# Performance work log

Measured on AMD Instinct MI355X. Metric: run time of the kernel, lower is better.

The kernel has to match this reference:

```python
import jax, jax.numpy as jnp
import numpy as np

EPS = 1e-10
ENTROPY_COEF = 0.1
COLSUM_COEF = 1.0


def setup_inputs() -> dict:
    key = jax.random.key(0)
    k1, k2, k3 = jax.random.split(key, 3)
    H, T, B, S = 512, 50003, 32, 256
    colsum_threshold = 0.5
    return {
        "text_input": jax.random.randint(k1, (B, S), 0, T, dtype=jnp.int32),
        "init_logits": jnp.zeros((H,), dtype=jnp.float32),
        "transition_logits": jax.random.normal(k2, (H, H), dtype=jnp.float32) * 0.1,
        "emission_logits": jax.random.normal(k3, (H, T), dtype=jnp.float32) * 0.1,
        "colsum_threshold": colsum_threshold,
    }


def reference(text_input, init_logits, transition_logits, emission_logits, colsum_threshold):
    # softmax-normalized HMM parameters
    text_pi = jax.nn.softmax(init_logits, axis=0)              # [H]
    text_A = jax.nn.softmax(transition_logits, axis=1)         # [H,H]
    text_B = jax.nn.softmax(emission_logits, axis=1)           # [H,T]

    log_pi = jnp.log(text_pi + EPS)                            # [H]
    log_A = jnpp = jnp.log(text_A + EPS)                       # [H,H]
    log_B = jnp.log(text_B + EPS)                              # [H,T]

    # gather per-token emission log-probs: [B,S,H]
    log_B_obs = log_B.T[text_input]

    # t = 0
    log_alpha0 = log_pi[None, :] + log_B_obs[:, 0, :]          # [B,H]

    def step(log_alpha, obs_t):
        # logsumexp over source state i: [B,H(i),1] + [1,H(i),H(j)] -> [B,H(j)]
        trans = log_alpha[:, :, None] + log_A[None, :, :]
        new_alpha = jax.nn.logsumexp(trans, axis=1) + obs_t
        return new_alpha, None

    obs_rest = jnp.swapaxes(log_B_obs[:, 1:, :], 0, 1)         # [S-1,B,H]
    log_alpha_final, _ = jax.lax.scan(step, log_alpha0, obs_rest)

    log_likelihood = jax.nn.logsumexp(log_alpha_final, axis=1)  # [B]
    likelihood_loss = -jnp.mean(log_likelihood)

    transition_entropy = -jnp.sum(text_A * jnp.log(text_A + EPS), axis=1)
    transition_entropy_loss = jnp.mean(transition_entropy) * ENTROPY_COEF

    col_sums = jnp.sum(text_A, axis=0)
    colsum_reg = jnp.sum(jax.nn.relu(colsum_threshold - col_sums)) * COLSUM_COEF

    hmm_loss = likelihood_loss + transition_entropy_loss + colsum_reg
    return text_pi, text_A, text_B, hmm_loss
```

## Files before the change

### kernel.cpp

```cpp
#include <hip/hip_runtime.h>
#include <hip/hip_bf16.h>
#include <stdint.h>

#define HH 512
#define BB 32
#define SSEQ 256
#define TVOC 50003
#define EPSF 1e-10f
#define EMSCALE 96.0f
#define TOTLOG 2759.2459164008406f

typedef float f32x4 __attribute__((ext_vector_type(4)));
typedef int v8i __attribute__((ext_vector_type(8)));

__device__ __forceinline__ float wave_max(float v) {
#pragma unroll
  for (int off = 32; off; off >>= 1) v = fmaxf(v, __shfl_xor(v, off));
  return v;
}
__device__ __forceinline__ float wave_sum(float v) {
#pragma unroll
  for (int off = 32; off; off >>= 1) v += __shfl_xor(v, off);
  return v;
}

__global__ __launch_bounds__(512) void init_ws_kernel(float* ws) {
  if (threadIdx.x < 8) ws[threadIdx.x] = 0.0f;
  ws[8 + threadIdx.x] = 0.0f;
}

__global__ __launch_bounds__(512) void softmax_pi_kernel(
    const float* __restrict__ x, float* __restrict__ pi) {
  const int tid = threadIdx.x;
  const int wv = tid >> 6, ln = tid & 63;
  __shared__ float red[8];
  float v = x[tid];
  float m = wave_max(v);
  if (ln == 0) red[wv] = m;
  __syncthreads();
  float M = red[0];
#pragma unroll
  for (int i = 1; i < 8; ++i) M = fmaxf(M, red[i]);
  float e = __expf(v - M);
  float s = wave_sum(e);
  __syncthreads();
  if (ln == 0) red[wv] = s;
  __syncthreads();
  float S = 0.f;
#pragma unroll
  for (int i = 0; i < 8; ++i) S += red[i];
  pi[tid] = e / S;
}

__global__ __launch_bounds__(512) void softmaxA_kernel(
    const float* __restrict__ tl, float* __restrict__ outA,
    float* __restrict__ ws_ent) {
  const int r = blockIdx.x, tid = threadIdx.x;
  const int wv = tid >> 6, ln = tid & 63;
  __shared__ float red[8];
  float v = tl[(size_t)r * HH + tid];
  float m = wave_max(v);
  if (ln == 0) red[wv] = m;
  __syncthreads();
  float M = red[0];
#pragma unroll
  for (int i = 1; i < 8; ++i) M = fmaxf(M, red[i]);
  float e = __expf(v - M);
  float s = wave_sum(e);
  __syncthreads();
  if (ln == 0) red[wv] = s;
  __syncthreads();
  float S = 0.f;
#pragma unroll
  for (int i = 0; i < 8; ++i) S += red[i];
  float p = e / S;
  outA[(size_t)r * HH + tid] = p;
  float ent = -p * __logf(p + EPSF);
  ent = wave_sum(ent);
  __syncthreads();
  if (ln == 0) red[wv] = ent;
  __syncthreads();
  if (tid == 0) {
    float tot = 0.f;
#pragma unroll
    for (int i = 0; i < 8; ++i) tot += red[i];
    atomicAdd(ws_ent, tot);
  }
}

__global__ __launch_bounds__(512) void colsum_partial_kernel(
    const float* __restrict__ outA, float* __restrict__ col) {
  const int j = threadIdx.x;
  const int i0 = blockIdx.x * 64;
  float s = 0.f;
#pragma unroll 4
  for (int i = i0; i < i0 + 64; ++i) s += outA[(size_t)i * HH + j];
  atomicAdd(&col[j], s);
}

__global__ __launch_bounds__(1024) void softmaxB_gather_kernel(
    const float* __restrict__ el, float* __restrict__ outB,
    const int* __restrict__ tok, __hip_bfloat16* __restrict__ ems) {
  const int r = blockIdx.x, tid = threadIdx.x;
  const float* x = el + (size_t)r * TVOC;
  float* yo = outB + (size_t)r * TVOC;
  const int mis = (int)(((16u - ((unsigned)(uintptr_t)x & 15u)) & 15u) >> 2);
  const int body = (TVOC - mis) >> 2;
  const int tailoff = mis + body * 4;

  float m0 = -1e30f, s0 = 0.f, m1 = -1e30f, s1 = 0.f;
  float m2 = -1e30f, s2 = 0.f, m3 = -1e30f, s3 = 0.f;
  auto upd = [](float& m, float& s, float v) {
    if (v > m) { s = s * __expf(m - v) + 1.f; m = v; }
    else       { s += __expf(v - m); }
  };
  if (tid < mis) upd(m0, s0, x[tid]);
  const float4* x4 = (const float4*)(x + mis);
  for (int i = tid; i < body; i += 1024) {
    float4 v = x4[i];
    upd(m0, s0, v.x); upd(m1, s1, v.y); upd(m2, s2, v.z); upd(m3, s3, v.w);
  }
  for (int i = tailoff + tid; i < TVOC; i += 1024) upd(m0, s0, x[i]);
  auto mrg = [](float& m, float& s, float om, float os) {
    float nm = fmaxf(m, om);
    s = s * __expf(m - nm) + os * __expf(om - nm);
    m = nm;
  };
  mrg(m0, s0, m1, s1); mrg(m2, s2, m3, s3); mrg(m0, s0, m2, s2);
  float m = m0, s = s0;

#pragma unroll
  for (int off = 32; off; off >>= 1) {
    float om = __shfl_down(m, off), os = __shfl_down(s, off);
    float nm = fmaxf(m, om);
    s = s * __expf(m - nm) + os * __expf(om - nm);
    m = nm;
  }
  __shared__ float sm[16], ssv[16];
  __shared__ float bM, biZ;
  if ((tid & 63) == 0) { sm[tid >> 6] = m; ssv[tid >> 6] = s; }
  __syncthreads();
  if (tid == 0) {
    float M = sm[0], S = ssv[0];
#pragma unroll
    for (int w = 1; w < 16; ++w) {
      float nm = fmaxf(M, sm[w]);
      S = S * __expf(M - nm) + ssv[w] * __expf(sm[w] - nm);
      M = nm;
    }
    bM = M; biZ = 1.f / S;
  }
  __syncthreads();
  const float M = bM, iZ = biZ;
  if (tid < mis) yo[tid] = __expf(x[tid] - M) * iZ;
  float4* y4 = (float4*)(yo + mis);
  for (int i = tid; i < body; i += 1024) {
    float4 v = x4[i];
    float4 o;
    o.x = __expf(v.x - M) * iZ;
    o.y = __expf(v.y - M) * iZ;
    o.z = __expf(v.z - M) * iZ;
    o.w = __expf(v.w - M) * iZ;
    y4[i] = o;
  }
  for (int i = tailoff + tid; i < TVOC; i += 1024)
    yo[i] = __expf(x[i] - M) * iZ;

  const float gs = EMSCALE * iZ;
  const int rg = r >> 2, rl = r & 3;
  for (int idx = tid; idx < BB * SSEQ; idx += 1024) {
    const int sq = idx >> 5, b = idx & 31;
    const int t = tok[b * SSEQ + sq];
    ems[((size_t)(sq * 128 + rg) * 32 + b) * 4 + rl] =
        __float2bfloat16(__expf(x[t] - M) * gs);
  }
}

__global__ __launch_bounds__(512, 2) void scan_kernel(
    const float* __restrict__ d_pi, const float* __restrict__ d_A,
    const __hip_bfloat16* __restrict__ ems, float* __restrict__ ws_negll) {
  const int h = blockIdx.x;
  const int tid = threadIdx.x;
  const int lane = tid & 63;
  const int wave = tid >> 6;
  const int l15 = lane & 15;
  const int quad = lane >> 4;
  const int bG = h * 16 + l15;

  __shared__ __align__(16) unsigned char alpha[2][16][528];
  __shared__ float wmax[8][17];
  __shared__ float wsum[8][17];
  __shared__ float ls[16];

  const unsigned short* emsu = (const unsigned short*)ems;
  const uint2* emv = (const uint2*)ems;

  v8i aF[4][4];
#pragma unroll
  for (int n = 0; n < 4; ++n) {
    const int jg = wave * 64 + n * 16 + l15;
#pragma unroll
    for (int c = 0; c < 4; ++c) {
#pragma unroll
      for (int g = 0; g < 8; ++g) {
        const int k0 = c * 128 + quad * 32 + g * 4;
        const float v0 = d_A[(size_t)(k0 + 0) * HH + jg] * 512.0f;
        const float v1 = d_A[(size_t)(k0 + 1) * HH + jg] * 512.0f;
        const float v2 = d_A[(size_t)(k0 + 2) * HH + jg] * 512.0f;
        const float v3 = d_A[(size_t)(k0 + 3) * HH + jg] * 512.0f;
        int wrd = 0;
        wrd = __builtin_amdgcn_cvt_pk_fp8_f32(v0, v1, wrd, false);
        wrd = __builtin_amdgcn_cvt_pk_fp8_f32(v2, v3, wrd, true);
        aF[n][c][g] = wrd;
      }
    }
  }

#pragma unroll
  for (int it = 0; it < 2; ++it) {
    const int b = wave * 2 + it;
    const int bb = h * 16 + b;
    const int j0 = lane * 8;
    float vals[8];
    float m = -1e30f;
#pragma unroll
    for (int u = 0; u < 8; ++u) {
      const int j = j0 + u;
      const unsigned ew = (unsigned)emsu[((size_t)(j >> 2) * 32 + bb) * 4 + (j & 3)] << 16;
      vals[u] = (d_pi[j] + EPSF) * __uint_as_float(ew);
      m = fmaxf(m, vals[u]);
    }
    m = wave_max(m);
    if (lane == 0) ls[b] = __logf(m);
    const float r = 1.0f / m;
    int lo = 0, hi = 0;
    lo = __builtin_amdgcn_cvt_pk_fp8_f32(vals[0] * r, vals[1] * r, lo, false);
    lo = __builtin_amdgcn_cvt_pk_fp8_f32(vals[2] * r, vals[3] * r, lo, true);
    hi = __builtin_amdgcn_cvt_pk_fp8_f32(vals[4] * r, vals[5] * r, hi, false);
    hi = __builtin_amdgcn_cvt_pk_fp8_f32(vals[6] * r, vals[7] * r, hi, true);
    *(unsigned int*)&alpha[0][b][j0]     = (unsigned)lo;
    *(unsigned int*)&alpha[0][b][j0 + 4] = (unsigned)hi;
  }
  __syncthreads();

  const uint2* ep = emv + ((size_t)1 * 128 + wave * 16 + quad) * 32 + bG;
  uint2 evr[4];
#pragma unroll
  for (int n = 0; n < 4; ++n) evr[n] = ep[n * 128];
  ep += 128 * 32;

#pragma unroll 2
  for (int t = 1; t < SSEQ; ++t) {
    const int cur = (t - 1) & 1, nxt = t & 1;

    float ev[4][4];
#pragma unroll
    for (int n = 0; n < 4; ++n) {
      ev[n][0] = __uint_as_float(evr[n].x << 16);
      ev[n][1] = __uint_as_float(evr[n].x & 0xFFFF0000u);
      ev[n][2] = __uint_as_float(evr[n].y << 16);
      ev[n][3] = __uint_as_float(evr[n].y & 0xFFFF0000u);
    }
#pragma unroll
    for (int n = 0; n < 4; ++n) evr[n] = ep[n * 128];
    if (t <= SSEQ - 3) ep += 128 * 32;

    f32x4 acc0 = {0.f, 0.f, 0.f, 0.f}, acc1 = {0.f, 0.f, 0.f, 0.f};
    f32x4 acc2 = {0.f, 0.f, 0.f, 0.f}, acc3 = {0.f, 0.f, 0.f, 0.f};
#pragma unroll
    for (int c = 0; c < 4; ++c) {
      const unsigned char* ap = &alpha[cur][l15][c * 128 + quad * 32];
      v8i bf;
      *(int4*)&bf       = *(const int4*)ap;
      *(((int4*)&bf)+1) = *(const int4*)(ap + 16);
      acc0 = __builtin_amdgcn_mfma_scale_f32_16x16x128_f8f6f4(
          aF[0][c], bf, acc0, 0, 0, 0, 0x7F7F7F7F, 0, 0x7F7F7F7F);
      acc1 = __builtin_amdgcn_mfma_scale_f32_16x16x128_f8f6f4(
          aF[1][c], bf, acc1, 0, 0, 0, 0x7F7F7F7F, 0, 0x7F7F7F7F);
      acc2 = __builtin_amdgcn_mfma_scale_f32_16x16x128_f8f6f4(
          aF[2][c], bf, acc2, 0, 0, 0, 0x7F7F7F7F, 0, 0x7F7F7F7F);
      acc3 = __builtin_amdgcn_mfma_scale_f32_16x16x128_f8f6f4(
          aF[3][c], bf, acc3, 0, 0, 0, 0x7F7F7F7F, 0, 0x7F7F7F7F);
    }

    float y[4][4];
#pragma unroll
    for (int rg = 0; rg < 4; ++rg) {
      y[0][rg] = acc0[rg] * ev[0][rg];
      y[1][rg] = acc1[rg] * ev[1][rg];
      y[2][rg] = acc2[rg] * ev[2][rg];
      y[3][rg] = acc3[rg] * ev[3][rg];
    }

    float r = 1.0f;
    if ((t & 15) == 0) {
      float mm = -1e30f;
#pragma unroll
      for (int n = 0; n < 4; ++n)
#pragma unroll
        for (int rg = 0; rg < 4; ++rg) mm = fmaxf(mm, y[n][rg]);
      mm = fmaxf(mm, __shfl_xor(mm, 16));
      mm = fmaxf(mm, __shfl_xor(mm, 32));
      if (lane < 16) wmax[wave][lane] = mm;
      __syncthreads();
      float m = wmax[0][l15];
#pragma unroll
      for (int w = 1; w < 8; ++w) m = fmaxf(m, wmax[w][l15]);
      r = 1.0f / m;
      if (tid < 16) ls[tid] += __logf(m);
    }

#pragma unroll
    for (int n = 0; n < 4; ++n) {
      int d = 0;
      d = __builtin_amdgcn_cvt_pk_fp8_f32(y[n][0] * r, y[n][1] * r, d, false);
      d = __builtin_amdgcn_cvt_pk_fp8_f32(y[n][2] * r, y[n][3] * r, d, true);
      *(unsigned int*)&alpha[nxt][l15][wave * 64 + n * 16 + quad * 4] = (unsigned)d;
    }
    if (t == SSEQ - 1) {
      float s = 0.f;
#pragma unroll
      for (int n = 0; n < 4; ++n) s += y[n][0] + y[n][1] + y[n][2] + y[n][3];
      s *= r;
      s += __shfl_xor(s, 16);
      s += __shfl_xor(s, 32);
      if (lane < 16) wsum[wave][lane] = s;
    }
    __syncthreads();
  }

  if (wave == 0 && lane < 16) {
    float s = 0.f;
#pragma unroll
    for (int w = 0; w < 8; ++w) s += wsum[w][lane];
    const float LL = __logf(s) + ls[lane] - TOTLOG;
    atomicAdd(ws_negll, -LL * (1.0f / 32.0f));
  }
}

__global__ __launch_bounds__(512) void finalize_kernel(
    const float* __restrict__ ws, const float* __restrict__ col,
    const float* __restrict__ thr, float* __restrict__ out_loss) {
  const int j = threadIdx.x;
  float v = fmaxf(thr[0] - col[j], 0.f);
  v = wave_sum(v);
  __shared__ float red[8];
  if ((j & 63) == 0) red[j >> 6] = v;
  __syncthreads();
  if (j == 0) {
    float creg = 0.f;
#pragma unroll
    for (int i = 0; i < 8; ++i) creg += red[i];
    out_loss[0] = ws[1] + ws[0] * (0.1f / 512.0f) + creg;
  }
}

extern "C" void kernel_launch(void* const* d_in, const int* in_sizes, int n_in,
                              void* d_out, int out_size, void* d_ws, size_t ws_size,
                              hipStream_t stream) {
  const int*   tok    = (const int*)d_in[0];
  const float* initl  = (const float*)d_in[1];
  const float* transl = (const float*)d_in[2];
  const float* eml    = (const float*)d_in[3];
  const float* thr    = (const float*)d_in[4];

  float* out      = (float*)d_out;
  float* out_pi   = out;
  float* out_A    = out + HH;
  float* out_B    = out + HH + (size_t)HH * HH;
  float* out_loss = out + HH + (size_t)HH * HH + (size_t)HH * TVOC;

  float* wsf = (float*)d_ws;
  float* col = wsf + 8;
  __hip_bfloat16* ems = (__hip_bfloat16*)((char*)d_ws + 4096);

  init_ws_kernel<<<1, 512, 0, stream>>>(wsf);
  softmax_pi_kernel<<<1, 512, 0, stream>>>(initl, out_pi);
  softmaxA_kernel<<<512, 512, 0, stream>>>(transl, out_A, wsf + 0);
  colsum_partial_kernel<<<8, 512, 0, stream>>>(out_A, col);
  softmaxB_gather_kernel<<<512, 1024, 0, stream>>>(eml, out_B, tok, ems);
  scan_kernel<<<2, 512, 0, stream>>>(out_pi, out_A, ems, wsf + 1);
  finalize_kernel<<<1, 512, 0, stream>>>(wsf, col, thr, out_loss);
}
```

Measured before the change: 665.5 us.

## Split scan kernel across 16 waves per block with half the output columns each

The sequential HMM forward scan block grows from 8 to 16 waves. Each wave now owns 32 destination states (two MFMA accumulators) instead of 64, which halves the per-wave MFMA chain and the register-resident fp8 transition fragments on each serial step. The init step is also reworked to use vectorized loads of pi and emissions. In exchange, each per-step __syncthreads and the periodic max reduction now span 16 waves.

```diff
diff --git a/kernel.cpp b/kernel.cpp
--- a/kernel.cpp
+++ b/kernel.cpp
@@ -176,7 +176,7 @@
   }
 }
 
-__global__ __launch_bounds__(512, 2) void scan_kernel(
+__global__ __launch_bounds__(1024) void scan_kernel(
     const float* __restrict__ d_pi, const float* __restrict__ d_A,
     const __hip_bfloat16* __restrict__ ems, float* __restrict__ ws_negll) {
   const int h = blockIdx.x;
@@ -188,17 +188,16 @@
   const int bG = h * 16 + l15;
 
   __shared__ __align__(16) unsigned char alpha[2][16][528];
-  __shared__ float wmax[8][17];
-  __shared__ float wsum[8][17];
+  __shared__ float wmax[16][17];
+  __shared__ float wsum[16][17];
   __shared__ float ls[16];
 
-  const unsigned short* emsu = (const unsigned short*)ems;
   const uint2* emv = (const uint2*)ems;
 
-  v8i aF[4][4];
-#pragma unroll
-  for (int n = 0; n < 4; ++n) {
-    const int jg = wave * 64 + n * 16 + l15;
+  v8i aF[2][4];
+#pragma unroll
+  for (int n = 0; n < 2; ++n) {
+    const int jg = wave * 32 + n * 16 + l15;
 #pragma unroll
     for (int c = 0; c < 4; ++c) {
 #pragma unroll
@@ -216,20 +215,35 @@
     }
   }
 
-#pragma unroll
-  for (int it = 0; it < 2; ++it) {
-    const int b = wave * 2 + it;
+  {
+    const int b = wave;
     const int bb = h * 16 + b;
     const int j0 = lane * 8;
+    const float4 p0 = *(const float4*)&d_pi[j0];
+    const float4 p1 = *(const float4*)&d_pi[j0 + 4];
+    const uint2 e0 = emv[(size_t)(2 * lane) * 32 + bb];
+    const uint2 e1 = emv[(size_t)(2 * lane + 1) * 32 + bb];
+    float em[8];
+    em[0] = __uint_as_float(e0.x << 16);
+    em[1] = __uint_as_float(e0.x & 0xFFFF0000u);
+    em[2] = __uint_as_float(e0.y << 16);
+    em[3] = __uint_as_float(e0.y & 0xFFFF0000u);
+    em[4] = __uint_as_float(e1.x << 16);
+    em[5] = __uint_as_float(e1.x & 0xFFFF0000u);
+    em[6] = __uint_as_float(e1.y << 16);
+    em[7] = __uint_as_float(e1.y & 0xFFFF0000u);
     float vals[8];
+    vals[0] = (p0.x + EPSF) * em[0];
+    vals[1] = (p0.y + EPSF) * em[1];
+    vals[2] = (p0.z + EPSF) * em[2];
+    vals[3] = (p0.w + EPSF) * em[3];
+    vals[4] = (p1.x + EPSF) * em[4];
+    vals[5] = (p1.y + EPSF) * em[5];
+    vals[6] = (p1.z + EPSF) * em[6];
+    vals[7] = (p1.w + EPSF) * em[7];
     float m = -1e30f;
 #pragma unroll
-    for (int u = 0; u < 8; ++u) {
-      const int j = j0 + u;
-      const unsigned ew = (unsigned)emsu[((size_t)(j >> 2) * 32 + bb) * 4 + (j & 3)] << 16;
-      vals[u] = (d_pi[j] + EPSF) * __uint_as_float(ew);
-      m = fmaxf(m, vals[u]);
-    }
+    for (int u = 0; u < 8; ++u) m = fmaxf(m, vals[u]);
     m = wave_max(m);
     if (lane == 0) ls[b] = __logf(m);
     const float r = 1.0f / m;
@@ -243,60 +257,53 @@
   }
   __syncthreads();
 
-  const uint2* ep = emv + ((size_t)1 * 128 + wave * 16 + quad) * 32 + bG;
-  uint2 evr[4];
-#pragma unroll
-  for (int n = 0; n < 4; ++n) evr[n] = ep[n * 128];
+  const uint2* ep = emv + ((size_t)1 * 128 + wave * 8 + quad) * 32 + bG;
+  uint2 evr[2];
+#pragma unroll
+  for (int n = 0; n < 2; ++n) evr[n] = ep[n * 128];
   ep += 128 * 32;
 
 #pragma unroll 2
   for (int t = 1; t < SSEQ; ++t) {
     const int cur = (t - 1) & 1, nxt = t & 1;
 
-    float ev[4][4];
-#pragma unroll
-    for (int n = 0; n < 4; ++n) {
+    float ev[2][4];
+#pragma unroll
+    for (int n = 0; n < 2; ++n) {
       ev[n][0] = __uint_as_float(evr[n].x << 16);
       ev[n][1] = __uint_as_float(evr[n].x & 0xFFFF0000u);
       ev[n][2] = __uint_as_float(evr[n].y << 16);
       ev[n][3] = __uint_as_float(evr[n].y & 0xFFFF0000u);
     }
 #pragma unroll
-    for (int n = 0; n < 4; ++n) evr[n] = ep[n * 128];
+    for (int n = 0; n < 2; ++n) evr[n] = ep[n * 128];
     if (t <= SSEQ - 3) ep += 128 * 32;
 
     f32x4 acc0 = {0.f, 0.f, 0.f, 0.f}, acc1 = {0.f, 0.f, 0.f, 0.f};
-    f32x4 acc2 = {0.f, 0.f, 0.f, 0.f}, acc3 = {0.f, 0.f, 0.f, 0.f};
 #pragma unroll
     for (int c = 0; c < 4; ++c) {
       const unsigned char* ap = &alpha[cur][l15][c * 128 + quad * 32];
       v8i bf;
-      *(int4*)&bf       = *(const int4*)ap;
-      *(((int4*)&bf)+1) = *(const int4*)(ap + 16);
+      *(int4*)&bf         = *(const int4*)ap;
+      *(((int4*)&bf) + 1) = *(const int4*)(ap + 16);
       acc0 = __builtin_amdgcn_mfma_scale_f32_16x16x128_f8f6f4(
           aF[0][c], bf, acc0, 0, 0, 0, 0x7F7F7F7F, 0, 0x7F7F7F7F);
       acc1 = __builtin_amdgcn_mfma_scale_f32_16x16x128_f8f6f4(
           aF[1][c], bf, acc1, 0, 0, 0, 0x7F7F7F7F, 0, 0x7F7F7F7F);
-      acc2 = __builtin_amdgcn_mfma_scale_f32_16x16x128_f8f6f4(
-          aF[2][c], bf, acc2, 0, 0, 0, 0x7F7F7F7F, 0, 0x7F7F7F7F);
-      acc3 = __builtin_amdgcn_mfma_scale_f32_16x16x128_f8f6f4(
-          aF[3][c], bf, acc3, 0, 0, 0, 0x7F7F7F7F, 0, 0x7F7F7F7F);
-    }
-
-    float y[4][4];
+    }
+
+    float y[2][4];
 #pragma unroll
     for (int rg = 0; rg < 4; ++rg) {
       y[0][rg] = acc0[rg] * ev[0][rg];
       y[1][rg] = acc1[rg] * ev[1][rg];
-      y[2][rg] = acc2[rg] * ev[2][rg];
-      y[3][rg] = acc3[rg] * ev[3][rg];
     }
 
     float r = 1.0f;
     if ((t & 15) == 0) {
       float mm = -1e30f;
 #pragma unroll
-      for (int n = 0; n < 4; ++n)
+      for (int n = 0; n < 2; ++n)
 #pragma unroll
         for (int rg = 0; rg < 4; ++rg) mm = fmaxf(mm, y[n][rg]);
       mm = fmaxf(mm, __shfl_xor(mm, 16));
@@ -305,23 +312,21 @@
       __syncthreads();
       float m = wmax[0][l15];
 #pragma unroll
-      for (int w = 1; w < 8; ++w) m = fmaxf(m, wmax[w][l15]);
+      for (int w = 1; w < 16; ++w) m = fmaxf(m, wmax[w][l15]);
       r = 1.0f / m;
       if (tid < 16) ls[tid] += __logf(m);
     }
 
 #pragma unroll
-    for (int n = 0; n < 4; ++n) {
+    for (int n = 0; n < 2; ++n) {
       int d = 0;
       d = __builtin_amdgcn_cvt_pk_fp8_f32(y[n][0] * r, y[n][1] * r, d, false);
       d = __builtin_amdgcn_cvt_pk_fp8_f32(y[n][2] * r, y[n][3] * r, d, true);
-      *(unsigned int*)&alpha[nxt][l15][wave * 64 + n * 16 + quad * 4] = (unsigned)d;
+      *(unsigned int*)&alpha[nxt][l15][wave * 32 + n * 16 + quad * 4] = (unsigned)d;
     }
     if (t == SSEQ - 1) {
-      float s = 0.f;
-#pragma unroll
-      for (int n = 0; n < 4; ++n) s += y[n][0] + y[n][1] + y[n][2] + y[n][3];
-      s *= r;
+      float s = (y[0][0] + y[0][1] + y[0][2] + y[0][3] +
+                 y[1][0] + y[1][1] + y[1][2] + y[1][3]) * r;
       s += __shfl_xor(s, 16);
       s += __shfl_xor(s, 32);
       if (lane < 16) wsum[wave][lane] = s;
@@ -332,7 +337,7 @@
   if (wave == 0 && lane < 16) {
     float s = 0.f;
 #pragma unroll
-    for (int w = 0; w < 8; ++w) s += wsum[w][lane];
+    for (int w = 0; w < 16; ++w) s += wsum[w][lane];
     const float LL = __logf(s) + ls[lane] - TOTLOG;
     atomicAdd(ws_negll, -LL * (1.0f / 32.0f));
   }
@@ -379,6 +384,6 @@
   softmaxA_kernel<<<512, 512, 0, stream>>>(transl, out_A, wsf + 0);
   colsum_partial_kernel<<<8, 512, 0, stream>>>(out_A, col);
   softmaxB_gather_kernel<<<512, 1024, 0, stream>>>(eml, out_B, tok, ems);
-  scan_kernel<<<2, 512, 0, stream>>>(out_pi, out_A, ems, wsf + 1);
+  scan_kernel<<<2, 1024, 0, stream>>>(out_pi, out_A, ems, wsf + 1);
   finalize_kernel<<<1, 512, 0, stream>>>(wsf, col, thr, out_loss);
 }
```

Result: faster. 573.9 us (-13.8%).
